# Optimization experiments

Measured on AMD Instinct MI355X. Metric: run time of the kernel, lower is better.

The kernel has to match this reference:

```python
import jax, jax.numpy as jnp
import numpy as np

ALPHA = 1.702
EPS_RMS = 1e-6
W_LOAD = 0.01
W_IMP = 0.01
W_AUX = 1.0
LIMIT = 7.0
K_TOP = 4


def swiglu(x, alpha=ALPHA, limit=LIMIT):
    x_glu = jnp.clip(x[..., ::2], -limit, limit)
    x_lin = jnp.clip(x[..., 1::2], -limit, limit)
    return x_glu * jax.nn.sigmoid(x_glu * alpha) + (x_lin + 1.0)


def setup_inputs() -> dict:
    key = jax.random.key(0)
    ks = jax.random.split(key, 4)
    T, H, I, E = 2048, 512, 512, 8
    x = jax.random.normal(ks[0], (T, H), dtype=jnp.float32)
    norm_scale = jnp.ones((H,), jnp.float32)
    gate_w = jax.random.normal(ks[1], (E, H), jnp.float32) * 0.02
    gate_b = jnp.zeros((E,), jnp.float32)
    mlp1_w = jax.random.normal(ks[2], (E, 2 * I, H), jnp.float32) * 0.02
    mlp1_b = jnp.zeros((E, 2 * I), jnp.float32)
    mlp2_w = jax.random.normal(ks[3], (E, H, I), jnp.float32) * 0.02
    mlp2_b = jnp.zeros((E, H), jnp.float32)
    return {"x": x, "norm_scale": norm_scale, "gate_w": gate_w, "gate_b": gate_b,
            "mlp1_w": mlp1_w, "mlp1_b": mlp1_b, "mlp2_w": mlp2_w, "mlp2_b": mlp2_b}


def reference(x, norm_scale, gate_w, gate_b, mlp1_w, mlp1_b, mlp2_w, mlp2_b):
    T, H = x.shape
    E = gate_w.shape[0]
    K = K_TOP
    # RMSNorm (fp32 math as in torch module)
    t = x * jax.lax.rsqrt(jnp.mean(x * x, axis=-1, keepdims=True) + EPS_RMS) * norm_scale
    # gating
    gate_logits = t @ gate_w.T + gate_b                      # [T, E]
    gate_probs = jax.nn.softmax(gate_logits, axis=-1)
    expert_weights, experts_indices = jax.lax.top_k(gate_probs, K)
    expert_weights = expert_weights / expert_weights.sum(axis=-1, keepdims=True)
    # per-token per-expert combine coefficient (sum of slot weights routed to e)
    coeff = jnp.zeros((T, E), x.dtype).at[jnp.arange(T)[:, None], experts_indices].add(expert_weights)
    # dense expert compute (math-equivalent to the gathered einsums; avoids
    # materializing per-token weight matrices)
    h = jnp.einsum('th,ech->tec', t, mlp1_w) + mlp1_b[None]  # [T, E, 2I]
    a = swiglu(h)                                            # [T, E, I]
    y = jnp.einsum('tei,ehi->teh', a, mlp2_w) + mlp2_b[None] # [T, E, H]
    out = jnp.einsum('teh,te->th', y, coeff) + x
    # aux losses (replicates the torch code exactly, incl. D-doubling quirk)
    P = gate_probs.mean(axis=0)                              # [E]
    counts = jax.vmap(lambda col: jnp.zeros((E,), x.dtype).at[col].add(1.0), in_axes=1)(experts_indices)  # [K, E]
    doubling = (2.0 ** (K - jnp.arange(K))).astype(x.dtype)  # D_i = 2*(D_{i-1}+c_i)
    D = (doubling[:, None] * counts).sum(axis=0) / (T * K)
    loss_load = W_LOAD * E * (P * D).sum()
    importance = gate_logits.sum(axis=0)
    cv = jnp.std(importance, ddof=1) / (importance.mean() + 1e-6)
    loss_imp = W_IMP * cv ** 2
    aux_loss = W_AUX * (loss_load + loss_imp)
    return out, aux_loss
```

## Files before the change

kernel.cpp:

```cpp
#include <hip/hip_runtime.h>
#include <stdint.h>

#define ALPHA 1.702f
#define LIMIT 7.0f

typedef float f32x4 __attribute__((ext_vector_type(4)));
typedef __bf16 bf16x8 __attribute__((ext_vector_type(8)));

static __device__ __forceinline__ unsigned short f2bf(float f) {
    union { float f; uint32_t u; } v; v.f = f;
    uint32_t u = v.u;
    return (unsigned short)((u + 0x7FFFu + ((u >> 16) & 1u)) >> 16);
}
static __device__ __forceinline__ int imin(int a, int b) { return a < b ? a : b; }

#define GLL16(GP, LP) __builtin_amdgcn_global_load_lds( \
    (const __attribute__((address_space(1))) void*)(GP), \
    (__attribute__((address_space(3))) void*)(LP), 16, 0, 0)

static __device__ __forceinline__ int lsw(int row, int kc) {
    return row * 4 + (kc ^ ((row >> 1) & 3));
}

__global__ __launch_bounds__(256) void prep_kernel(
    const float* __restrict__ w1,
    unsigned short* __restrict__ w1p,
    const float* __restrict__ x,
    const float* __restrict__ norm_scale,
    const float* __restrict__ gate_w,
    const float* __restrict__ gate_b,
    unsigned short* __restrict__ t_bf,
    int* __restrict__ pcnt,
    int* __restrict__ gtok,
    float* __restrict__ gwt,
    unsigned int* __restrict__ esel,
    float* __restrict__ cw4,
    float* __restrict__ paux)
{
    __shared__ float red[4][48];
    __shared__ int   ltok[8][8];
    __shared__ float lwt[8][8];
    __shared__ int   lcnt[8];
    if (blockIdx.x < 4096) {
        const int i4 = blockIdx.x * 256 + threadIdx.x;
        const int e = i4 >> 17;
        const int rem = i4 & 131071;
        const int r = rem >> 7;
        const int c = rem & 127;
        const int src = (r < 512) ? (2 * r) : (2 * (r - 512) + 1);
        float4 v = ((const float4*)w1)[(e << 17) + (src << 7) + c];
        ushort4 o = { f2bf(v.x), f2bf(v.y), f2bf(v.z), f2bf(v.w) };
        ((ushort4*)w1p)[i4] = o;
        return;
    }
    const int bid = blockIdx.x - 4096;
    const int wave = threadIdx.x >> 6;
    const int lane = threadIdx.x & 63;
    if (threadIdx.x < 8) lcnt[threadIdx.x] = 0;
    __syncthreads();

    float accP[8], accI[8], accC[32];
    #pragma unroll
    for (int e = 0; e < 8; ++e) { accP[e] = 0.f; accI[e] = 0.f; }
    #pragma unroll
    for (int i = 0; i < 32; ++i) accC[i] = 0.f;

    #pragma unroll
    for (int it = 0; it < 2; ++it) {
        const int t = bid * 8 + wave * 2 + it;
        const float4* xr = (const float4*)(x + t * 512);
        float4 x0 = xr[lane * 2];
        float4 x1 = xr[lane * 2 + 1];
        float ss = x0.x*x0.x + x0.y*x0.y + x0.z*x0.z + x0.w*x0.w
                 + x1.x*x1.x + x1.y*x1.y + x1.z*x1.z + x1.w*x1.w;
        #pragma unroll
        for (int off = 32; off > 0; off >>= 1) ss += __shfl_xor(ss, off, 64);
        const float rstd = rsqrtf(ss * (1.f / 512.f) + 1e-6f);
        const float4* sr = (const float4*)norm_scale;
        float4 s0 = sr[lane * 2], s1 = sr[lane * 2 + 1];
        float tv[8];
        tv[0] = x0.x * rstd * s0.x; tv[1] = x0.y * rstd * s0.y;
        tv[2] = x0.z * rstd * s0.z; tv[3] = x0.w * rstd * s0.w;
        tv[4] = x1.x * rstd * s1.x; tv[5] = x1.y * rstd * s1.y;
        tv[6] = x1.z * rstd * s1.z; tv[7] = x1.w * rstd * s1.w;
        uint32_t p0 = (uint32_t)f2bf(tv[0]) | ((uint32_t)f2bf(tv[1]) << 16);
        uint32_t p1 = (uint32_t)f2bf(tv[2]) | ((uint32_t)f2bf(tv[3]) << 16);
        uint32_t p2 = (uint32_t)f2bf(tv[4]) | ((uint32_t)f2bf(tv[5]) << 16);
        uint32_t p3 = (uint32_t)f2bf(tv[6]) | ((uint32_t)f2bf(tv[7]) << 16);
        uint4 pk; pk.x = p0; pk.y = p1; pk.z = p2; pk.w = p3;
        ((uint4*)(t_bf + t * 512))[lane] = pk;
        float le[8];
        #pragma unroll
        for (int e = 0; e < 8; ++e) {
            const float4* gw = (const float4*)(gate_w + e * 512);
            float4 g0 = gw[lane * 2], g1 = gw[lane * 2 + 1];
            float d = tv[0]*g0.x + tv[1]*g0.y + tv[2]*g0.z + tv[3]*g0.w
                    + tv[4]*g1.x + tv[5]*g1.y + tv[6]*g1.z + tv[7]*g1.w;
            #pragma unroll
            for (int off = 32; off > 0; off >>= 1) d += __shfl_xor(d, off, 64);
            le[e] = d + gate_b[e];
        }
        float mx = le[0];
        #pragma unroll
        for (int e = 1; e < 8; ++e) mx = fmaxf(mx, le[e]);
        float pe[8], se = 0.f;
        #pragma unroll
        for (int e = 0; e < 8; ++e) { pe[e] = __expf(le[e] - mx); se += pe[e]; }
        const float sinv = 1.f / se;
        #pragma unroll
        for (int e = 0; e < 8; ++e) pe[e] *= sinv;
        unsigned picked = 0;
        int ik[4]; float wk[4];
        #pragma unroll
        for (int k = 0; k < 4; ++k) {
            float bv = -1.f; int bi = 0;
            #pragma unroll
            for (int e = 0; e < 8; ++e)
                if (!(picked & (1u << e)) && pe[e] > bv) { bv = pe[e]; bi = e; }
            ik[k] = bi; wk[k] = bv; picked |= (1u << bi);
        }
        const float winv = 1.f / (wk[0] + wk[1] + wk[2] + wk[3]);
        float nw[4];
        #pragma unroll
        for (int k = 0; k < 4; ++k) nw[k] = wk[k] * winv;
        if (lane == 0) {
            #pragma unroll
            for (int k = 0; k < 4; ++k) {
                const int e = ik[k];
                const int pos = atomicAdd(&lcnt[e], 1);
                ltok[e][pos] = t; lwt[e][pos] = nw[k];
            }
            esel[t] = (unsigned)ik[0] | ((unsigned)ik[1] << 8)
                    | ((unsigned)ik[2] << 16) | ((unsigned)ik[3] << 24);
            float4 cwv; cwv.x = nw[0]; cwv.y = nw[1]; cwv.z = nw[2]; cwv.w = nw[3];
            ((float4*)cw4)[t] = cwv;
        }
        #pragma unroll
        for (int e = 0; e < 8; ++e) { accP[e] += pe[e]; accI[e] += le[e]; }
        #pragma unroll
        for (int k = 0; k < 4; ++k)
            #pragma unroll
            for (int e = 0; e < 8; ++e)
                accC[k * 8 + e] += (ik[k] == e) ? 1.f : 0.f;
    }
    if (lane == 0) {
        #pragma unroll
        for (int e = 0; e < 8; ++e) { red[wave][e] = accP[e]; red[wave][8 + e] = accI[e]; }
        #pragma unroll
        for (int i = 0; i < 32; ++i) red[wave][16 + i] = accC[i];
    }
    __syncthreads();
    if (threadIdx.x < 8) pcnt[bid * 8 + threadIdx.x] = lcnt[threadIdx.x];
    if (threadIdx.x < 64) {
        const int e = threadIdx.x >> 3, i = threadIdx.x & 7;
        if (i < lcnt[e]) {
            gtok[bid * 64 + threadIdx.x] = ltok[e][i];
            gwt[bid * 64 + threadIdx.x]  = lwt[e][i];
        }
    }
    if (threadIdx.x < 48) {
        paux[bid * 48 + threadIdx.x] =
            red[0][threadIdx.x] + red[1][threadIdx.x]
          + red[2][threadIdx.x] + red[3][threadIdx.x];
    }
}

__global__ __launch_bounds__(256, 2) void gemm1_swiglu(
    const unsigned short* __restrict__ A,
    const unsigned short* __restrict__ w1p,
    const float* __restrict__ b1,
    const int* __restrict__ pcnt,
    const int* __restrict__ gtok,
    const float* __restrict__ gwt,
    unsigned short* __restrict__ As,
    int* __restrict__ cntg,
    int* __restrict__ invslot,
    const float* __restrict__ paux,
    float* __restrict__ aux_out,
    const float* __restrict__ w2,
    unsigned short* __restrict__ w2b)
{
    if (blockIdx.x == 512) {
        __shared__ float sred[4][48];
        const int wv = threadIdx.x >> 6, ln = threadIdx.x & 63;
        if (ln < 48) {
            float s = 0.f;
            for (int b = 0; b < 64; ++b) s += paux[(wv * 64 + b) * 48 + ln];
            sred[wv][ln] = s;
        }
        __syncthreads();
        if (threadIdx.x == 0) {
            float imp[8], sl = 0.f;
            #pragma unroll
            for (int e = 0; e < 8; ++e) {
                float a0 = sred[0][e] + sred[1][e] + sred[2][e] + sred[3][e];
                float P = a0 * (1.f / 2048.f);
                imp[e] = sred[0][8+e] + sred[1][8+e] + sred[2][8+e] + sred[3][8+e];
                float c0 = sred[0][16+e] + sred[1][16+e] + sred[2][16+e] + sred[3][16+e];
                float c1 = sred[0][24+e] + sred[1][24+e] + sred[2][24+e] + sred[3][24+e];
                float c2 = sred[0][32+e] + sred[1][32+e] + sred[2][32+e] + sred[3][32+e];
                float c3 = sred[0][40+e] + sred[1][40+e] + sred[2][40+e] + sred[3][40+e];
                float D = (16.f * c0 + 8.f * c1 + 4.f * c2 + 2.f * c3) * (1.f / 8192.f);
                sl += P * D;
            }
            float loss_load = 0.01f * 8.f * sl;
            float mean = 0.f;
            #pragma unroll
            for (int e = 0; e < 8; ++e) mean += imp[e];
            mean *= 0.125f;
            float var = 0.f;
            #pragma unroll
            for (int e = 0; e < 8; ++e) { float d = imp[e] - mean; var += d * d; }
            var *= (1.f / 7.f);
            float cv = sqrtf(var) / (mean + 1e-6f);
            *aux_out = loss_load + 0.01f * cv * cv;
        }
        return;
    }
    if (blockIdx.x > 512) {
        const int i2 = (blockIdx.x - 513) * 256 + threadIdx.x;
        float4 v = ((const float4*)w2)[i2];
        ushort4 o = { f2bf(v.x), f2bf(v.y), f2bf(v.z), f2bf(v.w) };
        ((ushort4*)w2b)[i2] = o;
        return;
    }
    __shared__ unsigned short tA[2][4096];
    __shared__ unsigned short tBg[2][4096];
    __shared__ unsigned short tBl[2][4096];
    __shared__ int sscan[256];
    __shared__ int stok[128];
    __shared__ float swt[128];
    const int bx = blockIdx.x;
    const int tid = threadIdx.x;
    const int e = bx & 7;
    const int slot = bx >> 3;
    const int tile_m = slot >> 2, tile_n = slot & 3;
    const int m0 = tile_m * 128, np = tile_n * 128;

    {
        const int v = pcnt[tid * 8 + e];
        sscan[tid] = v;
        __syncthreads();
        for (int ofs = 1; ofs < 256; ofs <<= 1) {
            int add = (tid >= ofs) ? sscan[tid - ofs] : 0;
            __syncthreads();
            sscan[tid] += add;
            __syncthreads();
        }
    }
    const int cnte = sscan[255];
    if (slot == 0 && tid == 0) cntg[e] = cnte;
    if (m0 >= cnte) return;
    if (tid < 128) {
        const int s = imin(m0 + tid, cnte - 1);
        int lo = 0, hi = 255;
        #pragma unroll
        for (int itb = 0; itb < 8; ++itb) {
            const int mid = (lo + hi) >> 1;
            if (sscan[mid] > s) hi = mid; else lo = mid + 1;
        }
        const int b = lo;
        const int excl = (b > 0) ? sscan[b - 1] : 0;
        stok[tid] = gtok[b * 64 + e * 8 + (s - excl)];
        swt[tid]  = gwt[b * 64 + e * 8 + (s - excl)];
    }
    __syncthreads();
    if (tile_n == 0 && tid < 128 && (m0 + tid) < cnte)
        invslot[e * 2048 + stok[tid]] = m0 + tid;

    const int lane = tid & 63, wave = tid >> 6;
    const int wm = (wave & 1) * 64, wn = (wave >> 1) * 64;
    const int quad = lane >> 4, l16 = lane & 15;
    const int srow = tid >> 2;
    const int soff = ((tid & 3) ^ ((tid >> 3) & 3)) * 8;

    const int tok0 = stok[srow];
    const int tok1 = stok[64 + srow];
    float cw[4][4];
    #pragma unroll
    for (int i = 0; i < 4; ++i)
        #pragma unroll
        for (int r = 0; r < 4; ++r)
            cw[i][r] = swt[wm + i * 16 + quad * 4 + r];

    const unsigned short* Ar0 = A + tok0 * 512 + soff;
    const unsigned short* Ar1 = A + tok1 * 512 + soff;
    const unsigned short* Bg = w1p + (e * 1024 + np) * 512;
    const unsigned short* Bg0 = Bg + srow * 512 + soff;
    const unsigned short* Bg1 = Bg + (64 + srow) * 512 + soff;
    const unsigned short* Bl0 = Bg0 + 512 * 512;
    const unsigned short* Bl1 = Bg1 + 512 * 512;

    int rA[4], rB[4];
    #pragma unroll
    for (int i = 0; i < 4; ++i) {
        rA[i] = lsw(wm + i * 16 + l16, quad) * 8;
        rB[i] = lsw(wn + i * 16 + l16, quad) * 8;
    }

    f32x4 accG[4][4], accL[4][4];
    #pragma unroll
    for (int i = 0; i < 4; ++i)
        #pragma unroll
        for (int j = 0; j < 4; ++j) {
            f32x4 z = {0.f, 0.f, 0.f, 0.f};
            accG[i][j] = z; accL[i][j] = z;
        }

#define STAGE1(s, k0) do { \
    GLL16(Ar0 + (k0), tA[s] + tid * 8); \
    GLL16(Ar1 + (k0), tA[s] + (tid + 256) * 8); \
    GLL16(Bg0 + (k0), tBg[s] + tid * 8); \
    GLL16(Bg1 + (k0), tBg[s] + (tid + 256) * 8); \
    GLL16(Bl0 + (k0), tBl[s] + tid * 8); \
    GLL16(Bl1 + (k0), tBl[s] + (tid + 256) * 8); \
} while (0)

    STAGE1(0, 0);
    STAGE1(1, 32);
    #pragma unroll
    for (int kt = 0; kt < 16; ++kt) {
        const int cur = kt & 1;
        if (kt < 15) asm volatile("s_waitcnt vmcnt(6)" ::: "memory");
        else         asm volatile("s_waitcnt vmcnt(0)" ::: "memory");
        asm volatile("s_barrier" ::: "memory");
        bf16x8 af[4], bg[4], bl[4];
        #pragma unroll
        for (int i = 0; i < 4; ++i) {
            af[i] = *(const bf16x8*)(tA[cur] + rA[i]);
            bg[i] = *(const bf16x8*)(tBg[cur] + rB[i]);
            bl[i] = *(const bf16x8*)(tBl[cur] + rB[i]);
        }
        asm volatile("s_waitcnt lgkmcnt(0)" ::: "memory");
        asm volatile("s_barrier" ::: "memory");
        if (kt < 14) STAGE1(cur, (kt + 2) * 32);
        #pragma unroll
        for (int i = 0; i < 4; ++i)
            #pragma unroll
            for (int j = 0; j < 4; ++j) {
                accG[i][j] = __builtin_amdgcn_mfma_f32_16x16x32_bf16(af[i], bg[j], accG[i][j], 0, 0, 0);
                accL[i][j] = __builtin_amdgcn_mfma_f32_16x16x32_bf16(af[i], bl[j], accL[i][j], 0, 0, 0);
            }
    }
#undef STAGE1

    #pragma unroll
    for (int j = 0; j < 4; ++j) {
        const int colp = np + wn + j * 16 + l16;
        const float bgv = b1[e * 1024 + 2 * colp];
        const float blv = b1[e * 1024 + 2 * colp + 1];
        #pragma unroll
        for (int i = 0; i < 4; ++i) {
            const int sb = m0 + wm + i * 16 + quad * 4;
            #pragma unroll
            for (int r = 0; r < 4; ++r) {
                const int s = sb + r;
                if (s < cnte) {
                    float g2 = fminf(fmaxf(accG[i][j][r] + bgv, -LIMIT), LIMIT);
                    float l2 = fminf(fmaxf(accL[i][j][r] + blv, -LIMIT), LIMIT);
                    float a = g2 / (1.f + __expf(-ALPHA * g2)) + l2 + 1.f;
                    a *= cw[i][r];
                    As[e * 1048576 + s * 512 + colp] = f2bf(a);
                }
            }
        }
    }
}

__global__ __launch_bounds__(256, 2) void gemm2(
    const unsigned short* __restrict__ As,
    const unsigned short* __restrict__ w2b,
    const int* __restrict__ cntg,
    float* __restrict__ y)
{
    __shared__ unsigned short tA[2][4096];
    __shared__ unsigned short tB[2][4096];
    const int bx = blockIdx.x;
    const int tid = threadIdx.x;
    const int e = bx & 7;
    const int slot = bx >> 3;
    const int tile_m = slot >> 2, tile_n = slot & 3;
    const int m0 = tile_m * 128, n0 = tile_n * 128;
    const int cnte = cntg[e];
    if (m0 >= cnte) return;

    const int lane = tid & 63, wave = tid >> 6;
    const int wm = (wave & 1) * 64, wn = (wave >> 1) * 64;
    const int quad = lane >> 4, l16 = lane & 15;
    const int srow = tid >> 2;
    const int soff = ((tid & 3) ^ ((tid >> 3) & 3)) * 8;

    const unsigned short* Ar0 = As + e * 1048576 + (m0 + srow) * 512 + soff;
    const unsigned short* Ar1 = As + e * 1048576 + (m0 + 64 + srow) * 512 + soff;
    const unsigned short* Bb  = w2b + e * 262144;
    const unsigned short* Br0 = Bb + (n0 + srow) * 512 + soff;
    const unsigned short* Br1 = Bb + (n0 + 64 + srow) * 512 + soff;

    int rA[4], rB[4];
    #pragma unroll
    for (int i = 0; i < 4; ++i) {
        rA[i] = lsw(wm + i * 16 + l16, quad) * 8;
        rB[i] = lsw(wn + i * 16 + l16, quad) * 8;
    }

    f32x4 acc[4][4];
    #pragma unroll
    for (int i = 0; i < 4; ++i)
        #pragma unroll
        for (int j = 0; j < 4; ++j) { f32x4 z = {0.f, 0.f, 0.f, 0.f}; acc[i][j] = z; }

#define STAGE2(s, k0) do { \
    GLL16(Ar0 + (k0), tA[s] + tid * 8); \
    GLL16(Ar1 + (k0), tA[s] + (tid + 256) * 8); \
    GLL16(Br0 + (k0), tB[s] + tid * 8); \
    GLL16(Br1 + (k0), tB[s] + (tid + 256) * 8); \
} while (0)

    STAGE2(0, 0);
    STAGE2(1, 32);
    #pragma unroll
    for (int kt = 0; kt < 16; ++kt) {
        const int cur = kt & 1;
        if (kt < 15) asm volatile("s_waitcnt vmcnt(4)" ::: "memory");
        else         asm volatile("s_waitcnt vmcnt(0)" ::: "memory");
        asm volatile("s_barrier" ::: "memory");
        bf16x8 af[4], bf[4];
        #pragma unroll
        for (int i = 0; i < 4; ++i) {
            af[i] = *(const bf16x8*)(tA[cur] + rA[i]);
            bf[i] = *(const bf16x8*)(tB[cur] + rB[i]);
        }
        asm volatile("s_waitcnt lgkmcnt(0)" ::: "memory");
        asm volatile("s_barrier" ::: "memory");
        if (kt < 14) STAGE2(cur, (kt + 2) * 32);
        #pragma unroll
        for (int i = 0; i < 4; ++i)
            #pragma unroll
            for (int j = 0; j < 4; ++j)
                acc[i][j] = __builtin_amdgcn_mfma_f32_16x16x32_bf16(af[i], bf[j], acc[i][j], 0, 0, 0);
    }
#undef STAGE2

    float* yb = y + e * 1048576;
    #pragma unroll
    for (int i = 0; i < 4; ++i) {
        const int sb = m0 + wm + i * 16 + quad * 4;
        #pragma unroll
        for (int r = 0; r < 4; ++r) {
            const int s = sb + r;
            #pragma unroll
            for (int j = 0; j < 4; ++j) {
                const int col = n0 + wn + j * 16 + l16;
                yb[s * 512 + col] = acc[i][j][r];
            }
        }
    }
}

__global__ __launch_bounds__(256) void combine_kernel(
    const float* __restrict__ x,
    const float* __restrict__ b2,
    const float* __restrict__ y,
    const int* __restrict__ invslot,
    const unsigned int* __restrict__ esel,
    const float* __restrict__ cw4,
    float* __restrict__ out)
{
    const int tid = threadIdx.x;
    const int lane = tid & 63, wave = tid >> 6;
    #pragma unroll
    for (int it = 0; it < 2; ++it) {
        const int t = blockIdx.x * 8 + wave * 2 + it;
        const float4* xr = (const float4*)(x + t * 512);
        float4 o0 = xr[lane * 2];
        float4 o1 = xr[lane * 2 + 1];
        const unsigned sel = esel[t];
        float4 cwv = ((const float4*)cw4)[t];
        const float cws[4] = { cwv.x, cwv.y, cwv.z, cwv.w };
        #pragma unroll
        for (int k = 0; k < 4; ++k) {
            const int e = (sel >> (8 * k)) & 255;
            const int s = invslot[e * 2048 + t];
            const float4* yr = (const float4*)(y + (e * 2048 + s) * 512);
            float4 y0 = yr[lane * 2], y1 = yr[lane * 2 + 1];
            const float4* br = (const float4*)(b2 + e * 512);
            float4 b0 = br[lane * 2], bb1 = br[lane * 2 + 1];
            const float c = cws[k];
            o0.x += y0.x + c * b0.x; o0.y += y0.y + c * b0.y;
            o0.z += y0.z + c * b0.z; o0.w += y0.w + c * b0.w;
            o1.x += y1.x + c * bb1.x; o1.y += y1.y + c * bb1.y;
            o1.z += y1.z + c * bb1.z; o1.w += y1.w + c * bb1.w;
        }
        float4* orow = (float4*)(out + t * 512);
        orow[lane * 2] = o0; orow[lane * 2 + 1] = o1;
    }
}

extern "C" void kernel_launch(void* const* d_in, const int* in_sizes, int n_in,
                              void* d_out, int out_size, void* d_ws, size_t ws_size,
                              hipStream_t stream)
{
    (void)in_sizes; (void)n_in; (void)out_size; (void)ws_size;
    const float* x          = (const float*)d_in[0];
    const float* norm_scale = (const float*)d_in[1];
    const float* gate_w     = (const float*)d_in[2];
    const float* gate_b     = (const float*)d_in[3];
    const float* mlp1_w     = (const float*)d_in[4];
    const float* mlp1_b     = (const float*)d_in[5];
    const float* mlp2_w     = (const float*)d_in[6];
    const float* mlp2_b     = (const float*)d_in[7];
    float* out = (float*)d_out;

    char* ws = (char*)d_ws;
    unsigned short* w1p   = (unsigned short*)(ws);
    unsigned short* w2b   = (unsigned short*)(ws + 8388608);
    unsigned short* tbf   = (unsigned short*)(ws + 12582912);
    unsigned short* As    = (unsigned short*)(ws + 14680064);
    float*          y     = (float*)(ws + 31457280);
    float*          paux  = (float*)(ws + 65011712);
    int*            pcnt  = (int*)(ws + 65060864);
    int*            gtok  = (int*)(ws + 65069056);
    float*          gwt   = (float*)(ws + 65134592);
    unsigned int*   esel  = (unsigned int*)(ws + 65200128);
    float*          cw4   = (float*)(ws + 65208320);
    int*            invsl = (int*)(ws + 65241088);
    int*            cntg  = (int*)(ws + 65306624);

    prep_kernel<<<4352, 256, 0, stream>>>(mlp1_w, w1p,
                                          x, norm_scale, gate_w, gate_b,
                                          tbf, pcnt, gtok, gwt, esel, cw4, paux);
    gemm1_swiglu<<<2561, 256, 0, stream>>>(tbf, w1p, mlp1_b, pcnt, gtok, gwt,
                                           As, cntg, invsl, paux,
                                           out + 2048 * 512, mlp2_w, w2b);
    gemm2<<<512, 256, 0, stream>>>(As, w2b, cntg, y);
    combine_kernel<<<256, 256, 0, stream>>>(x, mlp2_b, y, invsl, esel, cw4, out);
}
```

Measured before the change: 144.2 us.

## Store gemm2 output in bf16 and coarsen weight-conversion blocks

The per-expert gemm2 output buffer y now holds bf16 values instead of fp32, and the combine kernel reads them as packed bf16 pairs that it widens to float. This halves the bytes written by gemm2 and read by combine. Separately, the w1 and w2 fp32-to-bf16 conversion blocks now each process two and four chunks, which reduces the grid sizes of prep_kernel and gemm1_swiglu. The cost is an extra bf16 rounding of expert outputs before the weighted sum, which loses some accuracy.

```diff
diff --git a/kernel.cpp b/kernel.cpp
--- a/kernel.cpp
+++ b/kernel.cpp
@@ -11,6 +11,12 @@
     union { float f; uint32_t u; } v; v.f = f;
     uint32_t u = v.u;
     return (unsigned short)((u + 0x7FFFu + ((u >> 16) & 1u)) >> 16);
+}
+static __device__ __forceinline__ float bflo(uint32_t w) {
+    union { uint32_t u; float f; } v; v.u = w << 16; return v.f;
+}
+static __device__ __forceinline__ float bfhi(uint32_t w) {
+    union { uint32_t u; float f; } v; v.u = w & 0xffff0000u; return v.f;
 }
 static __device__ __forceinline__ int imin(int a, int b) { return a < b ? a : b; }
 
@@ -41,19 +47,22 @@
     __shared__ int   ltok[8][8];
     __shared__ float lwt[8][8];
     __shared__ int   lcnt[8];
-    if (blockIdx.x < 4096) {
-        const int i4 = blockIdx.x * 256 + threadIdx.x;
-        const int e = i4 >> 17;
-        const int rem = i4 & 131071;
-        const int r = rem >> 7;
-        const int c = rem & 127;
-        const int src = (r < 512) ? (2 * r) : (2 * (r - 512) + 1);
-        float4 v = ((const float4*)w1)[(e << 17) + (src << 7) + c];
-        ushort4 o = { f2bf(v.x), f2bf(v.y), f2bf(v.z), f2bf(v.w) };
-        ((ushort4*)w1p)[i4] = o;
+    if (blockIdx.x < 2048) {
+        #pragma unroll
+        for (int k = 0; k < 2; ++k) {
+            const int i4 = (blockIdx.x * 2 + k) * 256 + threadIdx.x;
+            const int e = i4 >> 17;
+            const int rem = i4 & 131071;
+            const int r = rem >> 7;
+            const int c = rem & 127;
+            const int src = (r < 512) ? (2 * r) : (2 * (r - 512) + 1);
+            float4 v = ((const float4*)w1)[(e << 17) + (src << 7) + c];
+            ushort4 o = { f2bf(v.x), f2bf(v.y), f2bf(v.z), f2bf(v.w) };
+            ((ushort4*)w1p)[i4] = o;
+        }
         return;
     }
-    const int bid = blockIdx.x - 4096;
+    const int bid = blockIdx.x - 2048;
     const int wave = threadIdx.x >> 6;
     const int lane = threadIdx.x & 63;
     if (threadIdx.x < 8) lcnt[threadIdx.x] = 0;
@@ -218,10 +227,14 @@
         return;
     }
     if (blockIdx.x > 512) {
-        const int i2 = (blockIdx.x - 513) * 256 + threadIdx.x;
-        float4 v = ((const float4*)w2)[i2];
-        ushort4 o = { f2bf(v.x), f2bf(v.y), f2bf(v.z), f2bf(v.w) };
-        ((ushort4*)w2b)[i2] = o;
+        const int base = (blockIdx.x - 513) * 1024 + threadIdx.x;
+        #pragma unroll
+        for (int k = 0; k < 4; ++k) {
+            const int i2 = base + k * 256;
+            float4 v = ((const float4*)w2)[i2];
+            ushort4 o = { f2bf(v.x), f2bf(v.y), f2bf(v.z), f2bf(v.w) };
+            ((ushort4*)w2b)[i2] = o;
+        }
         return;
     }
     __shared__ unsigned short tA[2][4096];
@@ -371,7 +384,7 @@
     const unsigned short* __restrict__ As,
     const unsigned short* __restrict__ w2b,
     const int* __restrict__ cntg,
-    float* __restrict__ y)
+    unsigned short* __restrict__ y)
 {
     __shared__ unsigned short tA[2][4096];
     __shared__ unsigned short tB[2][4096];
@@ -441,7 +454,7 @@
     }
 #undef STAGE2
 
-    float* yb = y + e * 1048576;
+    unsigned short* yb = y + e * 1048576;
     #pragma unroll
     for (int i = 0; i < 4; ++i) {
         const int sb = m0 + wm + i * 16 + quad * 4;
@@ -451,7 +464,7 @@
             #pragma unroll
             for (int j = 0; j < 4; ++j) {
                 const int col = n0 + wn + j * 16 + l16;
-                yb[s * 512 + col] = acc[i][j][r];
+                yb[s * 512 + col] = f2bf(acc[i][j][r]);
             }
         }
     }
@@ -460,7 +473,7 @@
 __global__ __launch_bounds__(256) void combine_kernel(
     const float* __restrict__ x,
     const float* __restrict__ b2,
-    const float* __restrict__ y,
+    const unsigned short* __restrict__ y,
     const int* __restrict__ invslot,
     const unsigned int* __restrict__ esel,
     const float* __restrict__ cw4,
@@ -481,15 +494,14 @@
         for (int k = 0; k < 4; ++k) {
             const int e = (sel >> (8 * k)) & 255;
             const int s = invslot[e * 2048 + t];
-            const float4* yr = (const float4*)(y + (e * 2048 + s) * 512);
-            float4 y0 = yr[lane * 2], y1 = yr[lane * 2 + 1];
+            uint4 p = ((const uint4*)(y + (e * 2048 + s) * 512))[lane];
             const float4* br = (const float4*)(b2 + e * 512);
             float4 b0 = br[lane * 2], bb1 = br[lane * 2 + 1];
             const float c = cws[k];
-            o0.x += y0.x + c * b0.x; o0.y += y0.y + c * b0.y;
-            o0.z += y0.z + c * b0.z; o0.w += y0.w + c * b0.w;
-            o1.x += y1.x + c * bb1.x; o1.y += y1.y + c * bb1.y;
-            o1.z += y1.z + c * bb1.z; o1.w += y1.w + c * bb1.w;
+            o0.x += bflo(p.x) + c * b0.x;  o0.y += bfhi(p.x) + c * b0.y;
+            o0.z += bflo(p.y) + c * b0.z;  o0.w += bfhi(p.y) + c * b0.w;
+            o1.x += bflo(p.z) + c * bb1.x; o1.y += bfhi(p.z) + c * bb1.y;
+            o1.z += bflo(p.w) + c * bb1.z; o1.w += bfhi(p.w) + c * bb1.w;
         }
         float4* orow = (float4*)(out + t * 512);
         orow[lane * 2] = o0; orow[lane * 2 + 1] = o1;
@@ -516,20 +528,20 @@
     unsigned short* w2b   = (unsigned short*)(ws + 8388608);
     unsigned short* tbf   = (unsigned short*)(ws + 12582912);
     unsigned short* As    = (unsigned short*)(ws + 14680064);
-    float*          y     = (float*)(ws + 31457280);
-    float*          paux  = (float*)(ws + 65011712);
-    int*            pcnt  = (int*)(ws + 65060864);
-    int*            gtok  = (int*)(ws + 65069056);
-    float*          gwt   = (float*)(ws + 65134592);
-    unsigned int*   esel  = (unsigned int*)(ws + 65200128);
-    float*          cw4   = (float*)(ws + 65208320);
-    int*            invsl = (int*)(ws + 65241088);
-    int*            cntg  = (int*)(ws + 65306624);
-
-    prep_kernel<<<4352, 256, 0, stream>>>(mlp1_w, w1p,
+    unsigned short* y     = (unsigned short*)(ws + 31457280);
+    float*          paux  = (float*)(ws + 48234496);
+    int*            pcnt  = (int*)(ws + 48283648);
+    int*            gtok  = (int*)(ws + 48291840);
+    float*          gwt   = (float*)(ws + 48357376);
+    unsigned int*   esel  = (unsigned int*)(ws + 48422912);
+    float*          cw4   = (float*)(ws + 48431104);
+    int*            invsl = (int*)(ws + 48463872);
+    int*            cntg  = (int*)(ws + 48529408);
+
+    prep_kernel<<<2304, 256, 0, stream>>>(mlp1_w, w1p,
                                           x, norm_scale, gate_w, gate_b,
                                           tbf, pcnt, gtok, gwt, esel, cw4, paux);
-    gemm1_swiglu<<<2561, 256, 0, stream>>>(tbf, w1p, mlp1_b, pcnt, gtok, gwt,
+    gemm1_swiglu<<<1025, 256, 0, stream>>>(tbf, w1p, mlp1_b, pcnt, gtok, gwt,
                                            As, cntg, invsl, paux,
                                            out + 2048 * 512, mlp2_w, w2b);
     gemm2<<<512, 256, 0, stream>>>(As, w2b, cntg, y);
```

Result: no change. 143.4 us (-0.6%).
